# Optimization experiments

Hardware: AMD Instinct MI355X
Metric: run time of the kernel (lower is better)

Reference implementation:

```python
import jax, jax.numpy as jnp
import numpy as np

B, D, L, E, RH, EH = 8192, 1024, 3, 8, 128, 256  # batch, dim, levels, experts, router hidden, expert hidden


def setup_inputs() -> dict:
    key = jax.random.key(0)
    ks = jax.random.split(key, 9)
    s_d = 1.0 / np.sqrt(D)
    s_rh = 1.0 / np.sqrt(RH)
    s_eh = 1.0 / np.sqrt(EH)
    return {
        "x": jax.random.normal(ks[0], (B, D), dtype=jnp.float32),
        # routers: Linear(D,128) -> ReLU -> Linear(128,E) -> softmax, one per level
        "router_w1": jax.random.uniform(ks[1], (L, D, RH), jnp.float32, -s_d, s_d),
        "router_b1": jax.random.uniform(ks[2], (L, RH), jnp.float32, -s_d, s_d),
        "router_w2": jax.random.uniform(ks[3], (L, RH, E), jnp.float32, -s_rh, s_rh),
        "router_b2": jax.random.uniform(ks[4], (L, E), jnp.float32, -s_rh, s_rh),
        # experts: Linear(D,256) -> ReLU -> Linear(256,D), E per level
        "expert_w1": jax.random.uniform(ks[5], (L, E, D, EH), jnp.float32, -s_d, s_d),
        "expert_b1": jax.random.uniform(ks[6], (L, E, EH), jnp.float32, -s_d, s_d),
        "expert_w2": jax.random.uniform(ks[7], (L, E, EH, D), jnp.float32, -s_eh, s_eh),
        "expert_b2": jax.random.uniform(ks[8], (L, E, D), jnp.float32, -s_eh, s_eh),
    }


def _forward(x, router_w1, router_b1, router_w2, router_b2,
             expert_w1, expert_b1, expert_w2, expert_b2):
    def level(cur, params):
        rw1, rb1, rw2, rb2, ew1, eb1, ew2, eb2 = params
        # router: [B,E] softmax weights
        rh = jax.nn.relu(cur @ rw1 + rb1)
        w = jax.nn.softmax(rh @ rw2 + rb2, axis=-1)
        # dense all-expert eval: grouped GEMMs
        h = jax.nn.relu(jnp.einsum("bd,edh->beh", cur, ew1) + eb1)  # [B,E,EH]
        y = jnp.einsum("beh,ehd->bed", h, ew2) + eb2                # [B,E,D]
        out = jnp.einsum("be,bed->bd", w, y)                        # softmax-weighted sum
        return out, None

    out, _ = jax.lax.scan(
        level, x,
        (router_w1, router_b1, router_w2, router_b2,
         expert_w1, expert_b1, expert_w2, expert_b2))
    return out


def reference(x, router_w1, router_b1, router_w2, router_b2,
              expert_w1, expert_b1, expert_w2, expert_b2):
    return _forward(x, router_w1, router_b1, router_w2, router_b2,
                    expert_w1, expert_b1, expert_w2, expert_b2)
```

## Files before the change

### kernel.cpp

```cpp
#include <hip/hip_runtime.h>
#include <stdint.h>

#define BB   8192
#define DD   1024
#define EE   8
#define RHH  128
#define EHH  256
#define NE1  2048
#define KX   2112

using f32x4  = __attribute__((ext_vector_type(4))) float;
using bf16x8 = __attribute__((ext_vector_type(8))) __bf16;

__device__ __forceinline__ unsigned short f2bf(float f) {
    union { float f; uint32_t u; } v; v.f = f;
    uint32_t u = v.u;
    uint32_t r = (u + 0x7FFFu + ((u >> 16) & 1u)) >> 16;
    return (unsigned short)r;
}
__device__ __forceinline__ float bf2f(unsigned short h) {
    union { uint32_t u; float f; } v; v.u = ((uint32_t)h) << 16;
    return v.f;
}

__device__ __forceinline__ void llds16(void* l, const void* g) {
    __builtin_amdgcn_global_load_lds(
        (const __attribute__((address_space(1))) uint32_t*)g,
        (__attribute__((address_space(3))) uint32_t*)l, 16, 0, 0);
}

__device__ __forceinline__ void rawbar() {
    asm volatile("" ::: "memory");
    __builtin_amdgcn_s_barrier();
    asm volatile("" ::: "memory");
}

template<int N> __device__ __forceinline__ void vmwait() {
    asm volatile("s_waitcnt vmcnt(%0)" :: "n"(N) : "memory");
}


__device__ __forceinline__ void prep_body(int pbid, int tid,
    const float* __restrict__ rw1, const float* __restrict__ ew1,
    const float* __restrict__ ew2, const float* __restrict__ eb2,
    unsigned short* __restrict__ rw1t, unsigned short* __restrict__ W1t,
    unsigned short* __restrict__ W2t)
{
    if (pbid < 512) {
        int o = pbid * 256 + tid;
        int h = o >> 10, d = o & 1023;
        rw1t[o] = f2bf(rw1[d * RHH + h]);
    } else if (pbid < 8704) {
        int o = (pbid - 512) * 256 + tid;
        int n = o >> 10, k = o & 1023;
        int e = n >> 8, hh = n & 255;
        W1t[o] = f2bf(ew1[((e << 10) + k) * 256 + hh]);
    } else {
        int o = (pbid - 8704) * 256 + tid;
        int d = o / KX;
        int np = o - d * KX;
        float v;
        if (np < NE1)            v = ew2[np * DD + d];
        else if (np < NE1 + EE)  v = eb2[(np - NE1) * DD + d];
        else                     v = 0.0f;
        W2t[o] = f2bf(v);
    }
}

__global__ __launch_bounds__(256) void mega0(
    const float* __restrict__ x, unsigned short* __restrict__ xb,
    unsigned short* __restrict__ Hb,
    const float* __restrict__ rw1, const float* __restrict__ ew1,
    const float* __restrict__ ew2, const float* __restrict__ eb2,
    unsigned short* __restrict__ rw1t, unsigned short* __restrict__ W1t,
    unsigned short* __restrict__ W2t)
{
    const int bid = blockIdx.x, tid = threadIdx.x;
    if (bid < 2048) {
        size_t idx = (size_t)bid * 256 + tid;
        const float* p = x + idx * 16;
        uint32_t w[8];
#pragma unroll
        for (int j = 0; j < 8; ++j) {
            f32x4 v;
            (void)v;
            w[j] = (uint32_t)f2bf(p[2 * j]) | ((uint32_t)f2bf(p[2 * j + 1]) << 16);
        }
        uint32_t* o = (uint32_t*)(xb + idx * 16);
        *(uint4*)(o)     = make_uint4(w[0], w[1], w[2], w[3]);
        *(uint4*)(o + 4) = make_uint4(w[4], w[5], w[6], w[7]);
    } else if (bid < 3840) {
        int idx = (bid - 2048) * 256 + tid;
        int row = idx / 56, j = idx - row * 56;
        Hb[(size_t)row * KX + NE1 + EE + j] = 0;
    } else {
        prep_body(bid - 3840, tid, rw1, ew1, ew2, eb2, rw1t, W1t, W2t);
    }
}

__global__ __launch_bounds__(256) void prep_all(
    const float* __restrict__ rw1, const float* __restrict__ ew1,
    const float* __restrict__ ew2, const float* __restrict__ eb2,
    unsigned short* __restrict__ rw1t, unsigned short* __restrict__ W1t,
    unsigned short* __restrict__ W2t)
{
    prep_body(blockIdx.x, threadIdx.x, rw1, ew1, ew2, eb2, rw1t, W1t, W2t);
}

__global__ __launch_bounds__(512, 2) void router_fused(
    const unsigned short* __restrict__ xb, const unsigned short* __restrict__ rw1t,
    const float* __restrict__ rw2, const float* __restrict__ rb1,
    const float* __restrict__ rb2, float* __restrict__ wbuf,
    unsigned short* __restrict__ Hb)
{
    __shared__ __align__(16) char SR[73728];

    const int tid = threadIdx.x;
    const int lane = tid & 63, wv = tid >> 6;
    const int g = wv >> 2, wq = wv & 3;
    const int l16 = lane & 15, lhi = lane >> 4;
    const long m0 = (long)blockIdx.x * 64;

    const int r0 = tid >> 2, sl = tid & 3;
    const int sg = sl ^ ((r0 >> 1) & 3);

    const int xrow = (tid >> 2) & 63, xkg = tid >> 8;
    const char* xsrc = (const char*)xb + (m0 + xrow) * 2048 + xkg * 1024 + sg * 16;
    const char* wsrc = (const char*)rw1t + (long)r0 * 2048 + sg * 16;

    f32x4 acc[8];
    const f32x4 zero = {0.f, 0.f, 0.f, 0.f};
#pragma unroll
    for (int i = 0; i < 8; ++i) acc[i] = zero;

    auto stage = [&](int buf, int t) {
        char* base = SR + buf * 24576;
        llds16(base + tid * 16, xsrc + t * 64);
        llds16(base + 8192 + tid * 16, wsrc + t * 64);
        llds16(base + 16384 + tid * 16, wsrc + 1024 + t * 64);
    };

    stage(0, 0); stage(1, 1);

    const int swz = (l16 >> 1) & 3;
    const int aoff = g * 2048 + (wq * 16 + l16) * 32 + ((lhi ^ swz) << 3);
    const int boff = 4096 + g * 4096 + l16 * 32 + ((lhi ^ swz) << 3);

    int cb = 0, sb = 2;
    for (int t = 0; t < 16; ++t) {
        if (t < 15) vmwait<3>(); else vmwait<0>();
        rawbar();
        const unsigned short* bufp = (const unsigned short*)(SR + cb * 24576);
        bf16x8 aF = *(const bf16x8*)&bufp[aoff];
        bf16x8 bF[8];
#pragma unroll
        for (int ni = 0; ni < 8; ++ni)
            bF[ni] = *(const bf16x8*)&bufp[boff + ni * 512];
        if (t + 2 < 16) stage(sb, t + 2);
        __builtin_amdgcn_s_setprio(1);
#pragma unroll
        for (int ni = 0; ni < 8; ++ni)
            acc[ni] = __builtin_amdgcn_mfma_f32_16x16x32_bf16(aF, bF[ni], acc[ni], 0, 0, 0);
        __builtin_amdgcn_s_setprio(0);
        cb = (cb + 1 == 3) ? 0 : cb + 1;
        sb = (sb + 1 == 3) ? 0 : sb + 1;
    }

    rawbar();

    float* rhs = (float*)SR;
    float* lg  = (float*)(SR + 64 * 132 * 4);

    if (g == 1) {
#pragma unroll
        for (int ni = 0; ni < 8; ++ni)
#pragma unroll
            for (int rr = 0; rr < 4; ++rr)
                rhs[(wq * 16 + lhi * 4 + rr) * 132 + ni * 16 + l16] = acc[ni][rr];
    }
    rawbar();
    if (g == 0) {
#pragma unroll
        for (int ni = 0; ni < 8; ++ni) {
            float bv = rb1[ni * 16 + l16];
#pragma unroll
            for (int rr = 0; rr < 4; ++rr) {
                int row = wq * 16 + lhi * 4 + rr, col = ni * 16 + l16;
                float v = acc[ni][rr] + rhs[row * 132 + col] + bv;
                rhs[row * 132 + col] = fmaxf(v, 0.f);
            }
        }
    }
    rawbar();

    {
        const int row = tid & 63, e = tid >> 6;
        float a2 = rb2[e];
        for (int h = 0; h < 128; ++h)
            a2 += rhs[row * 132 + h] * rw2[h * 8 + e];
        lg[row * 9 + e] = a2;
    }
    rawbar();

    if (tid < 64) {
        const int row = tid;
        float l[8], m = -1e30f;
#pragma unroll
        for (int e = 0; e < 8; ++e) { l[e] = lg[row * 9 + e]; m = fmaxf(m, l[e]); }
        float s = 0.f;
#pragma unroll
        for (int e = 0; e < 8; ++e) { l[e] = expf(l[e] - m); s += l[e]; }
        float inv = 1.f / s;
        const long gr = m0 + row;
#pragma unroll
        for (int e = 0; e < 8; ++e) {
            float w = l[e] * inv;
            wbuf[gr * 8 + e] = w;
            Hb[gr * KX + NE1 + e] = f2bf(w);
        }
    }
}

template<int BNv, int BKv, int NBUF, int WNv, int EPI>
__global__ __launch_bounds__(512, 2)
void gemmT(const unsigned short* __restrict__ A, const unsigned short* __restrict__ Bt,
           void* __restrict__ C, const float* __restrict__ bias,
           const float* __restrict__ wrow,
           int K, int lda, int ldb, int ldc)
{
    constexpr int KH  = BKv / 32;
    constexpr int WMv = 8 / WNv;
    constexpr int MR  = 256 / WMv;
    constexpr int NC  = BNv / WNv;
    constexpr int MI  = MR / 16;
    constexpr int NI  = NC / 16;
    constexpr int NCH = 16 / MI;
    constexpr int ALP = 2;
    constexpr int BLP = (BNv * 64) / 8192;
    constexpr int LPT = KH * (ALP + BLP);
    constexpr int SD  = NBUF - 1;
    constexpr int AKH = 256 * 32;
    constexpr int BKH = BNv * 32;

    __shared__ __align__(16) unsigned short As[NBUF * KH * AKH];
    __shared__ __align__(16) unsigned short Bs[NBUF * KH * BKH];

    const int tid = threadIdx.x;
    const int lane = tid & 63, wv = tid >> 6;
    const int wr = wv / WNv, wc = wv % WNv;
    const int l16 = lane & 15, lhi = lane >> 4;
    const long bm0 = (long)blockIdx.x * 256;
    const long bn0 = (long)blockIdx.y * BNv;

    const int r0 = tid >> 2, sl = tid & 3;
    const int sg = sl ^ ((r0 >> 1) & 3);

    const char* aSrc[ALP];
    const char* bSrc[BLP];
#pragma unroll
    for (int a = 0; a < ALP; ++a)
        aSrc[a] = (const char*)A + (bm0 + a * 128 + r0) * (long)lda * 2 + sg * 16;
#pragma unroll
    for (int b = 0; b < BLP; ++b)
        bSrc[b] = (const char*)Bt + (bn0 + b * 128 + r0) * (long)ldb * 2 + sg * 16;

    f32x4 acc[MI][NI];
    const f32x4 zero = {0.f, 0.f, 0.f, 0.f};
#pragma unroll
    for (int i = 0; i < MI; ++i)
#pragma unroll
        for (int j = 0; j < NI; ++j)
            acc[i][j] = zero;

    auto stage = [&](int buf, int t) {
        const int cbyte = t * (BKv * 2);
#pragma unroll
        for (int kh = 0; kh < KH; ++kh) {
            char* ad = (char*)As + ((buf * KH + kh) * AKH) * 2 + tid * 16;
            char* bd = (char*)Bs + ((buf * KH + kh) * BKH) * 2 + tid * 16;
#pragma unroll
            for (int a = 0; a < ALP; ++a)
                llds16(ad + a * 8192, aSrc[a] + cbyte + kh * 64);
#pragma unroll
            for (int b = 0; b < BLP; ++b)
                llds16(bd + b * 8192, bSrc[b] + cbyte + kh * 64);
        }
    };

    const int nt = K / BKv;
#pragma unroll
    for (int p = 0; p < SD; ++p) stage(p, p);

    const int swz = (l16 >> 1) & 3;
    const int aoff = (wr * MR + l16) * 32 + ((lhi ^ swz) << 3);
    const int boff = (wc * NC + l16) * 32 + ((lhi ^ swz) << 3);

    int cb = 0, sb = SD % NBUF;
    for (int t = 0; t < nt; ++t) {
        const int rem = nt - 1 - t;
        if (rem >= SD - 1) vmwait<LPT * (SD - 1)>();
        else if constexpr (SD >= 3) {
            if (rem == 1) vmwait<LPT>(); else vmwait<0>();
        } else vmwait<0>();
        rawbar();

        bf16x8 aF[KH][MI], bF[KH][NI];
#pragma unroll
        for (int kh = 0; kh < KH; ++kh) {
            const unsigned short* ap = &As[(cb * KH + kh) * AKH];
            const unsigned short* bp = &Bs[(cb * KH + kh) * BKH];
#pragma unroll
            for (int mi = 0; mi < MI; ++mi)
                aF[kh][mi] = *(const bf16x8*)&ap[aoff + mi * 512];
#pragma unroll
            for (int ni = 0; ni < NI; ++ni)
                bF[kh][ni] = *(const bf16x8*)&bp[boff + ni * 512];
        }

        if (t + SD < nt) stage(sb, t + SD);

#pragma unroll
        for (int kh = 0; kh < KH; ++kh) {
#pragma unroll
            for (int nc0 = 0; nc0 < NI; nc0 += NCH) {
                __builtin_amdgcn_s_setprio(1);
#pragma unroll
                for (int mi = 0; mi < MI; ++mi)
#pragma unroll
                    for (int nj = 0; nj < NCH; ++nj)
                        acc[mi][nc0 + nj] = __builtin_amdgcn_mfma_f32_16x16x32_bf16(
                            aF[kh][mi], bF[kh][nc0 + nj], acc[mi][nc0 + nj], 0, 0, 0);
                __builtin_amdgcn_s_setprio(0);
            }
        }

        cb = (cb + 1 == NBUF) ? 0 : cb + 1;
        sb = (sb + 1 == NBUF) ? 0 : sb + 1;
    }

#pragma unroll
    for (int mi = 0; mi < MI; ++mi) {
#pragma unroll
        for (int ni = 0; ni < NI; ++ni) {
            const long gn = bn0 + wc * NC + ni * 16 + l16;
            float bv = 0.f;
            if (EPI == 1) bv = bias[gn];
#pragma unroll
            for (int rr = 0; rr < 4; ++rr) {
                const long gm = bm0 + wr * MR + mi * 16 + lhi * 4 + rr;
                float v = acc[mi][ni][rr];
                if (EPI == 1) {
                    v = fmaxf(v + bv, 0.f) * wrow[gm * 8 + (int)(gn >> 8)];
                    ((unsigned short*)C)[gm * (long)ldc + gn] = f2bf(v);
                } else if (EPI == 2) {
                    ((unsigned short*)C)[gm * (long)ldc + gn] = f2bf(v);
                } else {
                    ((float*)C)[gm * (long)ldc + gn] = v;
                }
            }
        }
    }
}


extern "C" void kernel_launch(void* const* d_in, const int* in_sizes, int n_in,
                              void* d_out, int out_size, void* d_ws, size_t ws_size,
                              hipStream_t stream) {
    (void)in_sizes; (void)n_in; (void)out_size; (void)ws_size;
    const float* x   = (const float*)d_in[0];
    const float* rw1 = (const float*)d_in[1];
    const float* rb1 = (const float*)d_in[2];
    const float* rw2 = (const float*)d_in[3];
    const float* rb2 = (const float*)d_in[4];
    const float* ew1 = (const float*)d_in[5];
    const float* eb1 = (const float*)d_in[6];
    const float* ew2 = (const float*)d_in[7];
    const float* eb2 = (const float*)d_in[8];

    char* ws = (char*)d_ws;
    unsigned short* xb   = (unsigned short*)(ws);
    float*          wbuf = (float*)         (ws + 16777216);
    unsigned short* Hb   = (unsigned short*)(ws + 17039360);
    unsigned short* rw1t = (unsigned short*)(ws + 51642368);
    unsigned short* W1t  = (unsigned short*)(ws + 51904512);
    unsigned short* W2t  = (unsigned short*)(ws + 56098816);

    mega0<<<20992, 256, 0, stream>>>(x, xb, Hb, rw1, ew1, ew2, eb2, rw1t, W1t, W2t);

    for (int l = 0; l < 3; ++l) {
        if (l > 0)
            prep_all<<<17152, 256, 0, stream>>>(rw1 + (size_t)l * DD * RHH,
                                                ew1 + (size_t)l * EE * DD * EHH,
                                                ew2 + (size_t)l * EE * EHH * DD,
                                                eb2 + (size_t)l * EE * DD,
                                                rw1t, W1t, W2t);

        router_fused<<<128, 512, 0, stream>>>(xb, rw1t,
                                              rw2 + (size_t)l * RHH * EE,
                                              rb1 + (size_t)l * RHH,
                                              rb2 + (size_t)l * EE, wbuf, Hb);

        gemmT<256, 32, 4, 4, 1><<<dim3(32, 8), 512, 0, stream>>>(
            xb, W1t, Hb, eb1 + (size_t)l * NE1, wbuf, DD, DD, DD, KX);

        if (l < 2)
            gemmT<128, 64, 3, 2, 2><<<dim3(32, 8), 512, 0, stream>>>(
                Hb, W2t, xb, nullptr, nullptr, KX, KX, KX, DD);
        else
            gemmT<128, 64, 3, 2, 3><<<dim3(32, 8), 512, 0, stream>>>(
                Hb, W2t, d_out, nullptr, nullptr, KX, KX, KX, DD);
    }
}
```

Before: 320.1 us.

## Replace GEMM mainloop with double-buffered, sub-tile interleaved load/compute schedule

Replaces the generic multi-buffer gemmT with gemmF. gemmF uses double buffering with BK=64 and splits each k-step into two or four MFMA phases. The refill of the freed LDS sub-tile (A or B halves) is issued between phases, with barriers and lgkmcnt waits placed explicitly. Warp layout is fixed at 2x4 with 128 rows per wave group, so the N=128 config moves from a 4x2 to a 2x4 wave arrangement. The aim is to overlap global->LDS traffic with MFMA work at finer granularity and cut LDS footprint. The cost is many more barriers per iteration and a fragile hand-written schedule.

```diff
diff --git a/kernel.cpp b/kernel.cpp
--- a/kernel.cpp
+++ b/kernel.cpp
@@ -38,6 +38,13 @@
 template<int N> __device__ __forceinline__ void vmwait() {
     asm volatile("s_waitcnt vmcnt(%0)" :: "n"(N) : "memory");
 }
+
+__device__ __forceinline__ void lgkm0sb() {
+    asm volatile("s_waitcnt lgkmcnt(0)" ::: "memory");
+    __builtin_amdgcn_sched_barrier(0);
+}
+
+#define MFMA16(a,b,c) __builtin_amdgcn_mfma_f32_16x16x32_bf16(a,b,c,0,0,0)
 
 
 __device__ __forceinline__ void prep_body(int pbid, int tid,
@@ -81,11 +88,8 @@
         const float* p = x + idx * 16;
         uint32_t w[8];
 #pragma unroll
-        for (int j = 0; j < 8; ++j) {
-            f32x4 v;
-            (void)v;
+        for (int j = 0; j < 8; ++j)
             w[j] = (uint32_t)f2bf(p[2 * j]) | ((uint32_t)f2bf(p[2 * j + 1]) << 16);
-        }
         uint32_t* o = (uint32_t*)(xb + idx * 16);
         *(uint4*)(o)     = make_uint4(w[0], w[1], w[2], w[3]);
         *(uint4*)(o + 4) = make_uint4(w[4], w[5], w[6], w[7]);
@@ -160,7 +164,7 @@
         __builtin_amdgcn_s_setprio(1);
 #pragma unroll
         for (int ni = 0; ni < 8; ++ni)
-            acc[ni] = __builtin_amdgcn_mfma_f32_16x16x32_bf16(aF, bF[ni], acc[ni], 0, 0, 0);
+            acc[ni] = MFMA16(aF, bF[ni], acc[ni]);
         __builtin_amdgcn_s_setprio(0);
         cb = (cb + 1 == 3) ? 0 : cb + 1;
         sb = (sb + 1 == 3) ? 0 : sb + 1;
@@ -221,125 +225,213 @@
     }
 }
 
-template<int BNv, int BKv, int NBUF, int WNv, int EPI>
+template<int BNv, int EPI>
 __global__ __launch_bounds__(512, 2)
-void gemmT(const unsigned short* __restrict__ A, const unsigned short* __restrict__ Bt,
+void gemmF(const unsigned short* __restrict__ A, const unsigned short* __restrict__ Bt,
            void* __restrict__ C, const float* __restrict__ bias,
            const float* __restrict__ wrow,
            int K, int lda, int ldb, int ldc)
 {
-    constexpr int KH  = BKv / 32;
-    constexpr int WMv = 8 / WNv;
-    constexpr int MR  = 256 / WMv;
-    constexpr int NC  = BNv / WNv;
-    constexpr int MI  = MR / 16;
+    constexpr int NC  = BNv / 4;
     constexpr int NI  = NC / 16;
-    constexpr int NCH = 16 / MI;
-    constexpr int ALP = 2;
-    constexpr int BLP = (BNv * 64) / 8192;
-    constexpr int LPT = KH * (ALP + BLP);
-    constexpr int SD  = NBUF - 1;
-    constexpr int AKH = 256 * 32;
     constexpr int BKH = BNv * 32;
 
-    __shared__ __align__(16) unsigned short As[NBUF * KH * AKH];
-    __shared__ __align__(16) unsigned short Bs[NBUF * KH * BKH];
+    __shared__ __align__(16) unsigned short As[2][16384];
+    __shared__ __align__(16) unsigned short Bs[2][2 * BKH];
 
     const int tid = threadIdx.x;
     const int lane = tid & 63, wv = tid >> 6;
-    const int wr = wv / WNv, wc = wv % WNv;
+    const int wr = wv >> 2, wc = wv & 3;
     const int l16 = lane & 15, lhi = lane >> 4;
+    const int lq = lane >> 2, ls = lane & 3;
+
     const long bm0 = (long)blockIdx.x * 256;
     const long bn0 = (long)blockIdx.y * BNv;
 
-    const int r0 = tid >> 2, sl = tid & 3;
-    const int sg = sl ^ ((r0 >> 1) & 3);
-
-    const char* aSrc[ALP];
-    const char* bSrc[BLP];
-#pragma unroll
-    for (int a = 0; a < ALP; ++a)
-        aSrc[a] = (const char*)A + (bm0 + a * 128 + r0) * (long)lda * 2 + sg * 16;
-#pragma unroll
-    for (int b = 0; b < BLP; ++b)
-        bSrc[b] = (const char*)Bt + (bn0 + b * 128 + r0) * (long)ldb * 2 + sg * 16;
-
-    f32x4 acc[MI][NI];
+    const int arb = (wv & 3) * 16 + (wv >> 2) * 128 + lq;
+    const int sgA = ls ^ ((arb >> 1) & 3);
+    const int brb = (BNv == 256) ? ((wv >> 1) * 64 + (wv & 1) * 16 + lq)
+                                 : (wv * 16 + lq);
+    const int sgB = ls ^ ((brb >> 1) & 3);
+
+    const char* aSrcU[2];
+    aSrcU[0] = (const char*)A + (bm0 + arb) * (long)lda * 2 + sgA * 16;
+    aSrcU[1] = aSrcU[0] + 64 * (long)lda * 2;
+    const char* bSrcU[2];
+    bSrcU[0] = (const char*)Bt + (bn0 + brb) * (long)ldb * 2 + sgB * 16;
+    bSrcU[1] = bSrcU[0] + 32 * (long)ldb * 2;
+
+    const int aDst0 = arb * 64 + ls * 16;
+    const int bDst0 = brb * 64 + ls * 16;
+
+    auto stA = [&](int buf, int mih, int t) {
+#pragma unroll
+        for (int g = 0; g < 2; ++g)
+            llds16((char*)As + buf * 32768 + g * 16384 + aDst0 + mih * 4096,
+                   aSrcU[mih] + (long)t * 128 + g * 64);
+    };
+    auto stB = [&](int buf, int nih, int t) {
+#pragma unroll
+        for (int g = 0; g < 2; ++g)
+            llds16((char*)Bs + buf * (4 * BKH) + g * (2 * BKH) + bDst0 + nih * 2048,
+                   bSrcU[nih] + (long)t * 128 + g * 64);
+    };
+
+    f32x4 acc[8][NI];
     const f32x4 zero = {0.f, 0.f, 0.f, 0.f};
 #pragma unroll
-    for (int i = 0; i < MI; ++i)
+    for (int i = 0; i < 8; ++i)
 #pragma unroll
         for (int j = 0; j < NI; ++j)
             acc[i][j] = zero;
 
-    auto stage = [&](int buf, int t) {
-        const int cbyte = t * (BKv * 2);
-#pragma unroll
-        for (int kh = 0; kh < KH; ++kh) {
-            char* ad = (char*)As + ((buf * KH + kh) * AKH) * 2 + tid * 16;
-            char* bd = (char*)Bs + ((buf * KH + kh) * BKH) * 2 + tid * 16;
-#pragma unroll
-            for (int a = 0; a < ALP; ++a)
-                llds16(ad + a * 8192, aSrc[a] + cbyte + kh * 64);
-#pragma unroll
-            for (int b = 0; b < BLP; ++b)
-                llds16(bd + b * 8192, bSrc[b] + cbyte + kh * 64);
+    const int swzo = (lhi ^ ((l16 >> 1) & 3)) << 3;
+    const int arow0 = (wr * 128 + l16) * 32 + swzo;
+    const int brow0 = (wc * NC + l16) * 32 + swzo;
+
+    const int nt = K / 64;
+
+    if constexpr (BNv == 256) {
+        stA(0, 0, 0); stA(0, 1, 0);
+        stB(0, 0, 0); stB(0, 1, 0);
+        stA(1, 0, 1); stA(1, 1, 1);
+    } else {
+        stB(0, 0, 0);
+        stA(0, 0, 0); stA(0, 1, 0);
+        stB(1, 0, 1);
+    }
+
+    bf16x8 aF[2][4], bF[2][NI];
+
+    for (int t = 0; t < nt; ++t) {
+        const int buf = t & 1;
+
+        if constexpr (BNv == 256) {
+            if (t == nt - 1) vmwait<0>(); else vmwait<4>();
+            rawbar();
+#pragma unroll
+            for (int kk = 0; kk < 2; ++kk)
+#pragma unroll
+                for (int mi = 0; mi < 4; ++mi)
+                    aF[kk][mi] = *(const bf16x8*)&As[buf][kk * 8192 + arow0 + mi * 512];
+#pragma unroll
+            for (int kk = 0; kk < 2; ++kk)
+#pragma unroll
+                for (int nj = 0; nj < 2; ++nj)
+                    bF[kk][nj] = *(const bf16x8*)&Bs[buf][kk * BKH + brow0 + nj * 512];
+            if (t + 1 < nt) stB(buf ^ 1, 0, t + 1);
+            lgkm0sb();
+            __builtin_amdgcn_s_setprio(1);
+#pragma unroll
+            for (int kk = 0; kk < 2; ++kk)
+#pragma unroll
+                for (int mi = 0; mi < 4; ++mi)
+#pragma unroll
+                    for (int nj = 0; nj < 2; ++nj)
+                        acc[mi][nj] = MFMA16(aF[kk][mi], bF[kk][nj], acc[mi][nj]);
+            __builtin_amdgcn_s_setprio(0);
+            rawbar();
+
+#pragma unroll
+            for (int kk = 0; kk < 2; ++kk)
+#pragma unroll
+                for (int nj = 0; nj < 2; ++nj)
+                    bF[kk][2 + nj] = *(const bf16x8*)&Bs[buf][kk * BKH + brow0 + (2 + nj) * 512];
+            if (t + 1 < nt) stB(buf ^ 1, 1, t + 1);
+            rawbar();
+            lgkm0sb();
+            __builtin_amdgcn_s_setprio(1);
+#pragma unroll
+            for (int kk = 0; kk < 2; ++kk)
+#pragma unroll
+                for (int mi = 0; mi < 4; ++mi)
+#pragma unroll
+                    for (int nj = 0; nj < 2; ++nj)
+                        acc[mi][2 + nj] = MFMA16(aF[kk][mi], bF[kk][2 + nj], acc[mi][2 + nj]);
+            __builtin_amdgcn_s_setprio(0);
+            rawbar();
+
+#pragma unroll
+            for (int kk = 0; kk < 2; ++kk)
+#pragma unroll
+                for (int mi = 0; mi < 4; ++mi)
+                    aF[kk][mi] = *(const bf16x8*)&As[buf][kk * 8192 + arow0 + 2048 + mi * 512];
+            if (t + 2 < nt) stA(buf, 0, t + 2);
+            rawbar();
+            lgkm0sb();
+            __builtin_amdgcn_s_setprio(1);
+#pragma unroll
+            for (int kk = 0; kk < 2; ++kk)
+#pragma unroll
+                for (int mi = 0; mi < 4; ++mi)
+#pragma unroll
+                    for (int nj = 0; nj < 2; ++nj)
+                        acc[4 + mi][nj] = MFMA16(aF[kk][mi], bF[kk][nj], acc[4 + mi][nj]);
+            __builtin_amdgcn_s_setprio(0);
+            rawbar();
+
+            if (t + 2 < nt) stA(buf, 1, t + 2);
+            rawbar();
+            lgkm0sb();
+            __builtin_amdgcn_s_setprio(1);
+#pragma unroll
+            for (int kk = 0; kk < 2; ++kk)
+#pragma unroll
+                for (int mi = 0; mi < 4; ++mi)
+#pragma unroll
+                    for (int nj = 0; nj < 2; ++nj)
+                        acc[4 + mi][2 + nj] = MFMA16(aF[kk][mi], bF[kk][2 + nj], acc[4 + mi][2 + nj]);
+            __builtin_amdgcn_s_setprio(0);
+            rawbar();
+        } else {
+            if (t == nt - 1) vmwait<0>(); else vmwait<2>();
+            rawbar();
+#pragma unroll
+            for (int kk = 0; kk < 2; ++kk)
+#pragma unroll
+                for (int mi = 0; mi < 4; ++mi)
+                    aF[kk][mi] = *(const bf16x8*)&As[buf][kk * 8192 + arow0 + mi * 512];
+#pragma unroll
+            for (int kk = 0; kk < 2; ++kk)
+#pragma unroll
+                for (int nj = 0; nj < 2; ++nj)
+                    bF[kk][nj] = *(const bf16x8*)&Bs[buf][kk * BKH + brow0 + nj * 512];
+            if (t + 1 < nt) { stA(buf ^ 1, 0, t + 1); stA(buf ^ 1, 1, t + 1); }
+            lgkm0sb();
+            __builtin_amdgcn_s_setprio(1);
+#pragma unroll
+            for (int kk = 0; kk < 2; ++kk)
+#pragma unroll
+                for (int mi = 0; mi < 4; ++mi)
+#pragma unroll
+                    for (int nj = 0; nj < 2; ++nj)
+                        acc[mi][nj] = MFMA16(aF[kk][mi], bF[kk][nj], acc[mi][nj]);
+            __builtin_amdgcn_s_setprio(0);
+            rawbar();
+
+#pragma unroll
+            for (int kk = 0; kk < 2; ++kk)
+#pragma unroll
+                for (int mi = 0; mi < 4; ++mi)
+                    aF[kk][mi] = *(const bf16x8*)&As[buf][kk * 8192 + arow0 + 2048 + mi * 512];
+            if (t + 2 < nt) stB(buf, 0, t + 2);
+            rawbar();
+            lgkm0sb();
+            __builtin_amdgcn_s_setprio(1);
+#pragma unroll
+            for (int kk = 0; kk < 2; ++kk)
+#pragma unroll
+                for (int mi = 0; mi < 4; ++mi)
+#pragma unroll
+                    for (int nj = 0; nj < 2; ++nj)
+                        acc[4 + mi][nj] = MFMA16(aF[kk][mi], bF[kk][nj], acc[4 + mi][nj]);
+            __builtin_amdgcn_s_setprio(0);
+            rawbar();
         }
-    };
-
-    const int nt = K / BKv;
-#pragma unroll
-    for (int p = 0; p < SD; ++p) stage(p, p);
-
-    const int swz = (l16 >> 1) & 3;
-    const int aoff = (wr * MR + l16) * 32 + ((lhi ^ swz) << 3);
-    const int boff = (wc * NC + l16) * 32 + ((lhi ^ swz) << 3);
-
-    int cb = 0, sb = SD % NBUF;
-    for (int t = 0; t < nt; ++t) {
-        const int rem = nt - 1 - t;
-        if (rem >= SD - 1) vmwait<LPT * (SD - 1)>();
-        else if constexpr (SD >= 3) {
-            if (rem == 1) vmwait<LPT>(); else vmwait<0>();
-        } else vmwait<0>();
-        rawbar();
-
-        bf16x8 aF[KH][MI], bF[KH][NI];
-#pragma unroll
-        for (int kh = 0; kh < KH; ++kh) {
-            const unsigned short* ap = &As[(cb * KH + kh) * AKH];
-            const unsigned short* bp = &Bs[(cb * KH + kh) * BKH];
-#pragma unroll
-            for (int mi = 0; mi < MI; ++mi)
-                aF[kh][mi] = *(const bf16x8*)&ap[aoff + mi * 512];
-#pragma unroll
-            for (int ni = 0; ni < NI; ++ni)
-                bF[kh][ni] = *(const bf16x8*)&bp[boff + ni * 512];
-        }
-
-        if (t + SD < nt) stage(sb, t + SD);
-
-#pragma unroll
-        for (int kh = 0; kh < KH; ++kh) {
-#pragma unroll
-            for (int nc0 = 0; nc0 < NI; nc0 += NCH) {
-                __builtin_amdgcn_s_setprio(1);
-#pragma unroll
-                for (int mi = 0; mi < MI; ++mi)
-#pragma unroll
-                    for (int nj = 0; nj < NCH; ++nj)
-                        acc[mi][nc0 + nj] = __builtin_amdgcn_mfma_f32_16x16x32_bf16(
-                            aF[kh][mi], bF[kh][nc0 + nj], acc[mi][nc0 + nj], 0, 0, 0);
-                __builtin_amdgcn_s_setprio(0);
-            }
-        }
-
-        cb = (cb + 1 == NBUF) ? 0 : cb + 1;
-        sb = (sb + 1 == NBUF) ? 0 : sb + 1;
-    }
-
-#pragma unroll
-    for (int mi = 0; mi < MI; ++mi) {
+    }
+
+#pragma unroll
+    for (int mi = 0; mi < 8; ++mi) {
 #pragma unroll
         for (int ni = 0; ni < NI; ++ni) {
             const long gn = bn0 + wc * NC + ni * 16 + l16;
@@ -347,7 +439,7 @@
             if (EPI == 1) bv = bias[gn];
 #pragma unroll
             for (int rr = 0; rr < 4; ++rr) {
-                const long gm = bm0 + wr * MR + mi * 16 + lhi * 4 + rr;
+                const long gm = bm0 + wr * 128 + mi * 16 + lhi * 4 + rr;
                 float v = acc[mi][ni][rr];
                 if (EPI == 1) {
                     v = fmaxf(v + bv, 0.f) * wrow[gm * 8 + (int)(gn >> 8)];
@@ -400,14 +492,14 @@
                                               rb1 + (size_t)l * RHH,
                                               rb2 + (size_t)l * EE, wbuf, Hb);
 
-        gemmT<256, 32, 4, 4, 1><<<dim3(32, 8), 512, 0, stream>>>(
+        gemmF<256, 1><<<dim3(32, 8), 512, 0, stream>>>(
             xb, W1t, Hb, eb1 + (size_t)l * NE1, wbuf, DD, DD, DD, KX);
 
         if (l < 2)
-            gemmT<128, 64, 3, 2, 2><<<dim3(32, 8), 512, 0, stream>>>(
+            gemmF<128, 2><<<dim3(32, 8), 512, 0, stream>>>(
                 Hb, W2t, xb, nullptr, nullptr, KX, KX, KX, DD);
         else
-            gemmT<128, 64, 3, 2, 3><<<dim3(32, 8), 512, 0, stream>>>(
+            gemmF<128, 3><<<dim3(32, 8), 512, 0, stream>>>(
                 Hb, W2t, d_out, nullptr, nullptr, KX, KX, KX, DD);
     }
 }
```

Measured after the change: 335.1 us. 1.05x slower.

## Replace generic GEMM with phase-scheduled ping-pong GEMMs using BK=128 stages

Applied to the files above, without the earlier changes.

Replaces the templated gemmT with two specialised kernels (256x256 and 256x128 tiles). Each K-step of 128 is split into barrier-delimited phases that interleave LDS fragment reads, global-to-LDS async loads and MFMA clusters over a double buffer. This is meant to hide load latency and keep the matrix units busy. To make the second GEMM's K a multiple of 128, the Hb padding grows from 2112 to 2176, which adds zero-fill work and shifts the workspace offsets. The risk is extra barriers and more padded K work.

```diff
diff --git a/kernel.cpp b/kernel.cpp
--- a/kernel.cpp
+++ b/kernel.cpp
@@ -7,7 +7,7 @@
 #define RHH  128
 #define EHH  256
 #define NE1  2048
-#define KX   2112
+#define KX   2176
 
 using f32x4  = __attribute__((ext_vector_type(4))) float;
 using bf16x8 = __attribute__((ext_vector_type(8))) __bf16;
@@ -38,6 +38,20 @@
 template<int N> __device__ __forceinline__ void vmwait() {
     asm volatile("s_waitcnt vmcnt(%0)" :: "n"(N) : "memory");
 }
+
+#define MFMA16(a,b,c) __builtin_amdgcn_mfma_f32_16x16x32_bf16(a,b,c,0,0,0)
+
+#define PH_MID() do { rawbar(); \
+    asm volatile("s_waitcnt lgkmcnt(0)" ::: "memory"); \
+    __builtin_amdgcn_s_setprio(1); } while (0)
+#define PH_END() do { __builtin_amdgcn_s_setprio(0); rawbar(); } while (0)
+#define PH_END_VM(N) do { __builtin_amdgcn_s_setprio(0); vmwait<N>(); rawbar(); } while (0)
+
+#define CLUST(AM, AN, AF, BF)                            \
+    _Pragma("unroll") for (int kk = 0; kk < 2; ++kk)     \
+    _Pragma("unroll") for (int mi = 0; mi < 4; ++mi)     \
+    _Pragma("unroll") for (int nj = 0; nj < 2; ++nj)     \
+        acc[(AM) + mi][(AN) + nj] = MFMA16(AF[kk][mi], BF[kk][nj], acc[(AM) + mi][(AN) + nj]);
 
 
 __device__ __forceinline__ void prep_body(int pbid, int tid,
@@ -81,20 +95,17 @@
         const float* p = x + idx * 16;
         uint32_t w[8];
 #pragma unroll
-        for (int j = 0; j < 8; ++j) {
-            f32x4 v;
-            (void)v;
+        for (int j = 0; j < 8; ++j)
             w[j] = (uint32_t)f2bf(p[2 * j]) | ((uint32_t)f2bf(p[2 * j + 1]) << 16);
-        }
         uint32_t* o = (uint32_t*)(xb + idx * 16);
         *(uint4*)(o)     = make_uint4(w[0], w[1], w[2], w[3]);
         *(uint4*)(o + 4) = make_uint4(w[4], w[5], w[6], w[7]);
-    } else if (bid < 3840) {
+    } else if (bid < 5888) {
         int idx = (bid - 2048) * 256 + tid;
-        int row = idx / 56, j = idx - row * 56;
+        int row = idx / 120, j = idx - row * 120;
         Hb[(size_t)row * KX + NE1 + EE + j] = 0;
     } else {
-        prep_body(bid - 3840, tid, rw1, ew1, ew2, eb2, rw1t, W1t, W2t);
+        prep_body(bid - 5888, tid, rw1, ew1, ew2, eb2, rw1t, W1t, W2t);
     }
 }
 
@@ -160,7 +171,7 @@
         __builtin_amdgcn_s_setprio(1);
 #pragma unroll
         for (int ni = 0; ni < 8; ++ni)
-            acc[ni] = __builtin_amdgcn_mfma_f32_16x16x32_bf16(aF, bF[ni], acc[ni], 0, 0, 0);
+            acc[ni] = MFMA16(aF, bF[ni], acc[ni]);
         __builtin_amdgcn_s_setprio(0);
         cb = (cb + 1 == 3) ? 0 : cb + 1;
         sb = (sb + 1 == 3) ? 0 : sb + 1;
@@ -221,145 +232,248 @@
     }
 }
 
-template<int BNv, int BKv, int NBUF, int WNv, int EPI>
+template<int EPI>
 __global__ __launch_bounds__(512, 2)
-void gemmT(const unsigned short* __restrict__ A, const unsigned short* __restrict__ Bt,
-           void* __restrict__ C, const float* __restrict__ bias,
-           const float* __restrict__ wrow,
-           int K, int lda, int ldb, int ldc)
+void gemm256(const unsigned short* __restrict__ A, const unsigned short* __restrict__ Bt,
+             void* __restrict__ C, const float* __restrict__ bias,
+             const float* __restrict__ wrow,
+             int K, int lda, int ldb, int ldc)
 {
-    constexpr int KH  = BKv / 32;
-    constexpr int WMv = 8 / WNv;
-    constexpr int MR  = 256 / WMv;
-    constexpr int NC  = BNv / WNv;
-    constexpr int MI  = MR / 16;
-    constexpr int NI  = NC / 16;
-    constexpr int NCH = 16 / MI;
-    constexpr int ALP = 2;
-    constexpr int BLP = (BNv * 64) / 8192;
-    constexpr int LPT = KH * (ALP + BLP);
-    constexpr int SD  = NBUF - 1;
-    constexpr int AKH = 256 * 32;
-    constexpr int BKH = BNv * 32;
-
-    __shared__ __align__(16) unsigned short As[NBUF * KH * AKH];
-    __shared__ __align__(16) unsigned short Bs[NBUF * KH * BKH];
+    __shared__ __align__(16) unsigned short As[2][16384];
+    __shared__ __align__(16) unsigned short Bs[2][16384];
 
     const int tid = threadIdx.x;
     const int lane = tid & 63, wv = tid >> 6;
-    const int wr = wv / WNv, wc = wv % WNv;
+    const int wr = wv >> 2, wc = wv & 3;
     const int l16 = lane & 15, lhi = lane >> 4;
+    const int lq = lane >> 2, ls = lane & 3;
+
     const long bm0 = (long)blockIdx.x * 256;
-    const long bn0 = (long)blockIdx.y * BNv;
-
-    const int r0 = tid >> 2, sl = tid & 3;
-    const int sg = sl ^ ((r0 >> 1) & 3);
-
-    const char* aSrc[ALP];
-    const char* bSrc[BLP];
-#pragma unroll
-    for (int a = 0; a < ALP; ++a)
-        aSrc[a] = (const char*)A + (bm0 + a * 128 + r0) * (long)lda * 2 + sg * 16;
-#pragma unroll
-    for (int b = 0; b < BLP; ++b)
-        bSrc[b] = (const char*)Bt + (bn0 + b * 128 + r0) * (long)ldb * 2 + sg * 16;
-
-    f32x4 acc[MI][NI];
+    const long bn0 = (long)blockIdx.y * 256;
+
+    const int arb = (wv & 3) * 16 + (wv >> 2) * 128 + lq;
+    const int sgA = ls ^ ((arb >> 1) & 3);
+    const int brb = (wv >> 1) * 64 + (wv & 1) * 16 + lq;
+    const int sgB = ls ^ ((brb >> 1) & 3);
+
+    const char* aSrcU[2];
+    aSrcU[0] = (const char*)A + (bm0 + arb) * (long)lda * 2 + sgA * 16;
+    aSrcU[1] = aSrcU[0] + 64 * (long)lda * 2;
+    const char* bSrcU[2];
+    bSrcU[0] = (const char*)Bt + (bn0 + brb) * (long)ldb * 2 + sgB * 16;
+    bSrcU[1] = bSrcU[0] + 32 * (long)ldb * 2;
+
+    const int aDst0 = arb * 64 + ls * 16;
+    const int bDst0 = brb * 64 + ls * 16;
+
+    auto stA = [&](int buf, int mih, int t) {
+#pragma unroll
+        for (int g = 0; g < 2; ++g)
+            llds16((char*)As + buf * 32768 + g * 16384 + aDst0 + mih * 4096,
+                   aSrcU[mih] + (long)t * 128 + g * 64);
+    };
+    auto stB = [&](int buf, int nih, int t) {
+#pragma unroll
+        for (int g = 0; g < 2; ++g)
+            llds16((char*)Bs + buf * 32768 + g * 16384 + bDst0 + nih * 2048,
+                   bSrcU[nih] + (long)t * 128 + g * 64);
+    };
+
+    f32x4 acc[8][4];
     const f32x4 zero = {0.f, 0.f, 0.f, 0.f};
 #pragma unroll
-    for (int i = 0; i < MI; ++i)
-#pragma unroll
-        for (int j = 0; j < NI; ++j)
+    for (int i = 0; i < 8; ++i)
+#pragma unroll
+        for (int j = 0; j < 4; ++j)
             acc[i][j] = zero;
 
-    auto stage = [&](int buf, int t) {
-        const int cbyte = t * (BKv * 2);
-#pragma unroll
-        for (int kh = 0; kh < KH; ++kh) {
-            char* ad = (char*)As + ((buf * KH + kh) * AKH) * 2 + tid * 16;
-            char* bd = (char*)Bs + ((buf * KH + kh) * BKH) * 2 + tid * 16;
-#pragma unroll
-            for (int a = 0; a < ALP; ++a)
-                llds16(ad + a * 8192, aSrc[a] + cbyte + kh * 64);
-#pragma unroll
-            for (int b = 0; b < BLP; ++b)
-                llds16(bd + b * 8192, bSrc[b] + cbyte + kh * 64);
-        }
-    };
-
-    const int nt = K / BKv;
-#pragma unroll
-    for (int p = 0; p < SD; ++p) stage(p, p);
-
-    const int swz = (l16 >> 1) & 3;
-    const int aoff = (wr * MR + l16) * 32 + ((lhi ^ swz) << 3);
-    const int boff = (wc * NC + l16) * 32 + ((lhi ^ swz) << 3);
-
-    int cb = 0, sb = SD % NBUF;
-    for (int t = 0; t < nt; ++t) {
-        const int rem = nt - 1 - t;
-        if (rem >= SD - 1) vmwait<LPT * (SD - 1)>();
-        else if constexpr (SD >= 3) {
-            if (rem == 1) vmwait<LPT>(); else vmwait<0>();
-        } else vmwait<0>();
-        rawbar();
-
-        bf16x8 aF[KH][MI], bF[KH][NI];
-#pragma unroll
-        for (int kh = 0; kh < KH; ++kh) {
-            const unsigned short* ap = &As[(cb * KH + kh) * AKH];
-            const unsigned short* bp = &Bs[(cb * KH + kh) * BKH];
-#pragma unroll
-            for (int mi = 0; mi < MI; ++mi)
-                aF[kh][mi] = *(const bf16x8*)&ap[aoff + mi * 512];
-#pragma unroll
-            for (int ni = 0; ni < NI; ++ni)
-                bF[kh][ni] = *(const bf16x8*)&bp[boff + ni * 512];
-        }
-
-        if (t + SD < nt) stage(sb, t + SD);
-
-#pragma unroll
-        for (int kh = 0; kh < KH; ++kh) {
-#pragma unroll
-            for (int nc0 = 0; nc0 < NI; nc0 += NCH) {
-                __builtin_amdgcn_s_setprio(1);
-#pragma unroll
-                for (int mi = 0; mi < MI; ++mi)
-#pragma unroll
-                    for (int nj = 0; nj < NCH; ++nj)
-                        acc[mi][nc0 + nj] = __builtin_amdgcn_mfma_f32_16x16x32_bf16(
-                            aF[kh][mi], bF[kh][nc0 + nj], acc[mi][nc0 + nj], 0, 0, 0);
-                __builtin_amdgcn_s_setprio(0);
-            }
-        }
-
-        cb = (cb + 1 == NBUF) ? 0 : cb + 1;
-        sb = (sb + 1 == NBUF) ? 0 : sb + 1;
-    }
-
-#pragma unroll
-    for (int mi = 0; mi < MI; ++mi) {
-#pragma unroll
-        for (int ni = 0; ni < NI; ++ni) {
-            const long gn = bn0 + wc * NC + ni * 16 + l16;
-            float bv = 0.f;
-            if (EPI == 1) bv = bias[gn];
+    const int swzo = (lhi ^ ((l16 >> 1) & 3)) << 3;
+    const int arow0 = (wr * 128 + l16) * 32 + swzo;
+    const int brow0 = (wc * 64 + l16) * 32 + swzo;
+
+#define RD_A6(DST, BUF, MIH)                                  \
+    _Pragma("unroll") for (int kk = 0; kk < 2; ++kk)          \
+    _Pragma("unroll") for (int mi = 0; mi < 4; ++mi)          \
+        DST[kk][mi] = *(const bf16x8*)&As[BUF][kk * 8192 + arow0 + (MIH) * 2048 + mi * 512];
+#define RD_B6(DST, BUF, NIH)                                  \
+    _Pragma("unroll") for (int kk = 0; kk < 2; ++kk)          \
+    _Pragma("unroll") for (int nj = 0; nj < 2; ++nj)          \
+        DST[kk][nj] = *(const bf16x8*)&Bs[BUF][kk * 8192 + brow0 + ((NIH) * 2 + nj) * 512];
+
+    bf16x8 aF[2][4], bn0F[2][2], bn1F[2][2];
+
+    stA(0, 0, 0); stB(0, 0, 0); stB(0, 1, 0); stA(0, 1, 0);
+    stA(1, 0, 1); stB(1, 0, 1); stB(1, 1, 1);
+    vmwait<6>(); rawbar();
+
+    const int nI = K / 128;
+    for (int i = 0; i < nI; ++i) {
+        const int t = 2 * i;
+        const bool last = (i == nI - 1);
+
+        RD_A6(aF, 0, 0);
+        RD_B6(bn0F, 0, 0);
+        stA(1, 1, t + 1);
+        PH_MID(); CLUST(0, 0, aF, bn0F); PH_END();
+        RD_B6(bn1F, 0, 1);
+        if (!last) stA(0, 0, t + 2);
+        PH_MID(); CLUST(0, 2, aF, bn1F); PH_END();
+        RD_A6(aF, 0, 1);
+        if (!last) stB(0, 0, t + 2);
+        PH_MID(); CLUST(4, 2, aF, bn1F); PH_END();
+        if (!last) stB(0, 1, t + 2);
+        PH_MID(); CLUST(4, 0, aF, bn0F);
+        if (last) { PH_END_VM(0); } else { PH_END_VM(6); }
+        RD_A6(aF, 1, 0);
+        RD_B6(bn0F, 1, 0);
+        if (!last) stA(0, 1, t + 2);
+        PH_MID(); CLUST(0, 0, aF, bn0F); PH_END();
+        RD_B6(bn1F, 1, 1);
+        if (!last) stA(1, 0, t + 3);
+        PH_MID(); CLUST(0, 2, aF, bn1F); PH_END();
+        RD_A6(aF, 1, 1);
+        if (!last) stB(1, 0, t + 3);
+        PH_MID(); CLUST(4, 2, aF, bn1F); PH_END();
+        if (!last) stB(1, 1, t + 3);
+        PH_MID(); CLUST(4, 0, aF, bn0F);
+        if (!last) { PH_END_VM(6); }
+        else       { __builtin_amdgcn_s_setprio(0); }
+    }
+
+#pragma unroll
+    for (int mi = 0; mi < 8; ++mi) {
+#pragma unroll
+        for (int ni = 0; ni < 4; ++ni) {
+            const long gn = bn0 + wc * 64 + ni * 16 + l16;
+            float bv = (EPI == 1) ? bias[gn] : 0.f;
 #pragma unroll
             for (int rr = 0; rr < 4; ++rr) {
-                const long gm = bm0 + wr * MR + mi * 16 + lhi * 4 + rr;
+                const long gm = bm0 + wr * 128 + mi * 16 + lhi * 4 + rr;
                 float v = acc[mi][ni][rr];
                 if (EPI == 1) {
                     v = fmaxf(v + bv, 0.f) * wrow[gm * 8 + (int)(gn >> 8)];
                     ((unsigned short*)C)[gm * (long)ldc + gn] = f2bf(v);
-                } else if (EPI == 2) {
+                } else {
                     ((unsigned short*)C)[gm * (long)ldc + gn] = f2bf(v);
-                } else {
-                    ((float*)C)[gm * (long)ldc + gn] = v;
                 }
             }
         }
     }
+#undef RD_A6
+#undef RD_B6
+}
+
+template<int EPI>
+__global__ __launch_bounds__(512, 2)
+void gemm128(const unsigned short* __restrict__ A, const unsigned short* __restrict__ Bt,
+             void* __restrict__ C, int K, int lda, int ldb, int ldc)
+{
+    __shared__ __align__(16) unsigned short As[2][16384];
+    __shared__ __align__(16) unsigned short Bs[2][8192];
+
+    const int tid = threadIdx.x;
+    const int lane = tid & 63, wv = tid >> 6;
+    const int wr = wv >> 2, wc = wv & 3;
+    const int l16 = lane & 15, lhi = lane >> 4;
+    const int lq = lane >> 2, ls = lane & 3;
+
+    const long bm0 = (long)blockIdx.x * 256;
+    const long bn0 = (long)blockIdx.y * 128;
+
+    const int arb = (wv & 3) * 16 + (wv >> 2) * 128 + lq;
+    const int sgA = ls ^ ((arb >> 1) & 3);
+    const int brb = wv * 16 + lq;
+    const int sgB = ls ^ ((brb >> 1) & 3);
+
+    const char* aSrcU[2];
+    aSrcU[0] = (const char*)A + (bm0 + arb) * (long)lda * 2 + sgA * 16;
+    aSrcU[1] = aSrcU[0] + 64 * (long)lda * 2;
+    const char* bSrc = (const char*)Bt + (bn0 + brb) * (long)ldb * 2 + sgB * 16;
+
+    const int aDst0 = arb * 64 + ls * 16;
+    const int bDst0 = brb * 64 + ls * 16;
+
+    auto stA = [&](int buf, int mih, int t) {
+#pragma unroll
+        for (int g = 0; g < 2; ++g)
+            llds16((char*)As + buf * 32768 + g * 16384 + aDst0 + mih * 4096,
+                   aSrcU[mih] + (long)t * 128 + g * 64);
+    };
+    auto stB2 = [&](int buf, int t) {
+#pragma unroll
+        for (int g = 0; g < 2; ++g)
+            llds16((char*)Bs + buf * 16384 + g * 8192 + bDst0,
+                   bSrc + (long)t * 128 + g * 64);
+    };
+
+    f32x4 acc[8][2];
+    const f32x4 zero = {0.f, 0.f, 0.f, 0.f};
+#pragma unroll
+    for (int i = 0; i < 8; ++i)
+#pragma unroll
+        for (int j = 0; j < 2; ++j)
+            acc[i][j] = zero;
+
+    const int swzo = (lhi ^ ((l16 >> 1) & 3)) << 3;
+    const int arow0 = (wr * 128 + l16) * 32 + swzo;
+    const int brow0 = (wc * 32 + l16) * 32 + swzo;
+
+#define RD_A4(DST, BUF, MIH)                                  \
+    _Pragma("unroll") for (int kk = 0; kk < 2; ++kk)          \
+    _Pragma("unroll") for (int mi = 0; mi < 4; ++mi)          \
+        DST[kk][mi] = *(const bf16x8*)&As[BUF][kk * 8192 + arow0 + (MIH) * 2048 + mi * 512];
+#define RD_B4(DST, BUF)                                       \
+    _Pragma("unroll") for (int kk = 0; kk < 2; ++kk)          \
+    _Pragma("unroll") for (int nj = 0; nj < 2; ++nj)          \
+        DST[kk][nj] = *(const bf16x8*)&Bs[BUF][kk * 4096 + brow0 + nj * 512];
+
+    bf16x8 aF[2][4], bF[2][2];
+
+    stA(0, 0, 0); stB2(0, 0); stA(0, 1, 0);
+    stA(1, 0, 1); stB2(1, 1);
+    vmwait<6>(); rawbar();
+
+    const int nI = K / 128;
+    for (int i = 0; i < nI; ++i) {
+        const int t = 2 * i;
+        const bool last = (i == nI - 1);
+
+        RD_A4(aF, 0, 0);
+        RD_B4(bF, 0);
+        stA(1, 1, t + 1);
+        PH_MID(); CLUST(0, 0, aF, bF); PH_END_VM(6);
+        RD_A4(aF, 0, 1);
+        if (!last) { stA(0, 0, t + 2); stB2(0, t + 2); }
+        PH_MID(); CLUST(4, 0, aF, bF);
+        if (last) { PH_END_VM(2); } else { PH_END_VM(6); }
+        RD_A4(aF, 1, 0);
+        RD_B4(bF, 1);
+        if (!last) stA(0, 1, t + 2);
+        PH_MID(); CLUST(0, 0, aF, bF);
+        if (last) { PH_END_VM(0); } else { PH_END_VM(6); }
+        RD_A4(aF, 1, 1);
+        if (!last) { stA(1, 0, t + 3); stB2(1, t + 3); }
+        PH_MID(); CLUST(4, 0, aF, bF);
+        if (!last) { PH_END_VM(6); }
+        else       { __builtin_amdgcn_s_setprio(0); }
+    }
+
+#pragma unroll
+    for (int mi = 0; mi < 8; ++mi) {
+#pragma unroll
+        for (int ni = 0; ni < 2; ++ni) {
+            const long gn = bn0 + wc * 32 + ni * 16 + l16;
+#pragma unroll
+            for (int rr = 0; rr < 4; ++rr) {
+                const long gm = bm0 + wr * 128 + mi * 16 + lhi * 4 + rr;
+                float v = acc[mi][ni][rr];
+                if (EPI == 2) ((unsigned short*)C)[gm * (long)ldc + gn] = f2bf(v);
+                else          ((float*)C)[gm * (long)ldc + gn] = v;
+            }
+        }
+    }
+#undef RD_A4
+#undef RD_B4
 }
 
 
@@ -381,15 +495,15 @@
     unsigned short* xb   = (unsigned short*)(ws);
     float*          wbuf = (float*)         (ws + 16777216);
     unsigned short* Hb   = (unsigned short*)(ws + 17039360);
-    unsigned short* rw1t = (unsigned short*)(ws + 51642368);
-    unsigned short* W1t  = (unsigned short*)(ws + 51904512);
-    unsigned short* W2t  = (unsigned short*)(ws + 56098816);
-
-    mega0<<<20992, 256, 0, stream>>>(x, xb, Hb, rw1, ew1, ew2, eb2, rw1t, W1t, W2t);
+    unsigned short* rw1t = (unsigned short*)(ws + 52690944);
+    unsigned short* W1t  = (unsigned short*)(ws + 52953088);
+    unsigned short* W2t  = (unsigned short*)(ws + 57147392);
+
+    mega0<<<23296, 256, 0, stream>>>(x, xb, Hb, rw1, ew1, ew2, eb2, rw1t, W1t, W2t);
 
     for (int l = 0; l < 3; ++l) {
         if (l > 0)
-            prep_all<<<17152, 256, 0, stream>>>(rw1 + (size_t)l * DD * RHH,
+            prep_all<<<17408, 256, 0, stream>>>(rw1 + (size_t)l * DD * RHH,
                                                 ew1 + (size_t)l * EE * DD * EHH,
                                                 ew2 + (size_t)l * EE * EHH * DD,
                                                 eb2 + (size_t)l * EE * DD,
@@ -400,14 +514,14 @@
                                               rb1 + (size_t)l * RHH,
                                               rb2 + (size_t)l * EE, wbuf, Hb);
 
-        gemmT<256, 32, 4, 4, 1><<<dim3(32, 8), 512, 0, stream>>>(
+        gemm256<1><<<dim3(32, 8), 512, 0, stream>>>(
             xb, W1t, Hb, eb1 + (size_t)l * NE1, wbuf, DD, DD, DD, KX);
 
         if (l < 2)
-            gemmT<128, 64, 3, 2, 2><<<dim3(32, 8), 512, 0, stream>>>(
-                Hb, W2t, xb, nullptr, nullptr, KX, KX, KX, DD);
+            gemm128<2><<<dim3(32, 8), 512, 0, stream>>>(
+                Hb, W2t, xb, KX, KX, KX, DD);
         else
-            gemmT<128, 64, 3, 2, 3><<<dim3(32, 8), 512, 0, stream>>>(
-                Hb, W2t, d_out, nullptr, nullptr, KX, KX, KX, DD);
-    }
-}
+            gemm128<3><<<dim3(32, 8), 512, 0, stream>>>(
+                Hb, W2t, d_out, KX, KX, KX, DD);
+    }
+}
```

Result: slower. 346.2 us (+8.2%).

## Tile weight-prep transposes through shared memory and vectorize padding writes

Applied to the files above, without the earlier changes.

Replaces the per-element strided transpose-and-convert of expert and router weights with 64x64 tiles staged through padded shared memory, so both the global reads and the bf16 writes are coalesced. Padding zeroing and the eb2 bias columns are now written as 16-byte vector stores, which cuts the prep grid from tens of thousands of blocks to about a thousand. The GEMM main loop also issues the next stage's async loads before reading fragments from LDS, for extra overlap. Each block now uses a small shared buffer and a barrier, and the loop reorder changes when buffer reuse happens relative to the LDS reads.

```diff
diff --git a/kernel.cpp b/kernel.cpp
--- a/kernel.cpp
+++ b/kernel.cpp
@@ -39,31 +39,72 @@
     asm volatile("s_waitcnt vmcnt(%0)" :: "n"(N) : "memory");
 }
 
-
-__device__ __forceinline__ void prep_body(int pbid, int tid,
+#define MFMA16(a,b,c) __builtin_amdgcn_mfma_f32_16x16x32_bf16(a,b,c,0,0,0)
+
+__device__ __forceinline__ void prep_lvl_body(float (*T)[65], int pbid, int tid,
     const float* __restrict__ rw1, const float* __restrict__ ew1,
     const float* __restrict__ ew2, const float* __restrict__ eb2,
     unsigned short* __restrict__ rw1t, unsigned short* __restrict__ W1t,
     unsigned short* __restrict__ W2t)
 {
+    const int hl = tid & 63, gq = tid >> 6;
     if (pbid < 512) {
-        int o = pbid * 256 + tid;
-        int h = o >> 10, d = o & 1023;
-        rw1t[o] = f2bf(rw1[d * RHH + h]);
-    } else if (pbid < 8704) {
-        int o = (pbid - 512) * 256 + tid;
-        int n = o >> 10, k = o & 1023;
-        int e = n >> 8, hh = n & 255;
-        W1t[o] = f2bf(ew1[((e << 10) + k) * 256 + hh]);
+        int e = pbid >> 6, kt = (pbid >> 2) & 15, ht = pbid & 3;
+        const float* src = ew1 + ((size_t)e << 18);
+#pragma unroll
+        for (int i = 0; i < 16; ++i) {
+            int kl = i * 4 + gq;
+            T[kl][hl] = src[(size_t)(kt * 64 + kl) * 256 + ht * 64 + hl];
+        }
+        __syncthreads();
+#pragma unroll
+        for (int i = 0; i < 16; ++i) {
+            int hl2 = i * 4 + gq;
+            int n = e * 256 + ht * 64 + hl2;
+            W1t[(size_t)n * 1024 + kt * 64 + hl] = f2bf(T[hl][hl2]);
+        }
+    } else if (pbid < 1024) {
+        int b2 = pbid - 512;
+        int npt = b2 >> 4, dt = b2 & 15;
+#pragma unroll
+        for (int i = 0; i < 16; ++i) {
+            int npl = i * 4 + gq;
+            T[npl][hl] = ew2[(size_t)(npt * 64 + npl) * 1024 + dt * 64 + hl];
+        }
+        __syncthreads();
+#pragma unroll
+        for (int i = 0; i < 16; ++i) {
+            int dl2 = i * 4 + gq;
+            int d = dt * 64 + dl2;
+            W2t[(size_t)d * KX + npt * 64 + hl] = f2bf(T[hl][dl2]);
+        }
+    } else if (pbid < 1056) {
+        int b2 = pbid - 1024;
+        int dt = b2 >> 1, ht = b2 & 1;
+#pragma unroll
+        for (int i = 0; i < 16; ++i) {
+            int dl = i * 4 + gq;
+            T[dl][hl] = rw1[(size_t)(dt * 64 + dl) * 128 + ht * 64 + hl];
+        }
+        __syncthreads();
+#pragma unroll
+        for (int i = 0; i < 16; ++i) {
+            int hl2 = i * 4 + gq;
+            int h = ht * 64 + hl2;
+            rw1t[(size_t)h * 1024 + dt * 64 + hl] = f2bf(T[hl][hl2]);
+        }
+    } else if (pbid < 1060) {
+        int d = (pbid - 1056) * 256 + tid;
+        unsigned short vv[8];
+#pragma unroll
+        for (int e = 0; e < 8; ++e) vv[e] = f2bf(eb2[(size_t)e * 1024 + d]);
+        *(uint4*)&W2t[(size_t)d * KX + NE1] = *(const uint4*)vv;
     } else {
-        int o = (pbid - 8704) * 256 + tid;
-        int d = o / KX;
-        int np = o - d * KX;
-        float v;
-        if (np < NE1)            v = ew2[np * DD + d];
-        else if (np < NE1 + EE)  v = eb2[(np - NE1) * DD + d];
-        else                     v = 0.0f;
-        W2t[o] = f2bf(v);
+        int d = (pbid - 1060) * 256 + tid;
+        uint4 z = make_uint4(0, 0, 0, 0);
+#pragma unroll
+        for (int j = 0; j < 7; ++j)
+            *(uint4*)&W2t[(size_t)d * KX + NE1 + 8 + j * 8] = z;
     }
 }
 
@@ -75,36 +116,38 @@
     unsigned short* __restrict__ rw1t, unsigned short* __restrict__ W1t,
     unsigned short* __restrict__ W2t)
 {
+    __shared__ float T[64][65];
     const int bid = blockIdx.x, tid = threadIdx.x;
     if (bid < 2048) {
         size_t idx = (size_t)bid * 256 + tid;
         const float* p = x + idx * 16;
         uint32_t w[8];
 #pragma unroll
-        for (int j = 0; j < 8; ++j) {
-            f32x4 v;
-            (void)v;
+        for (int j = 0; j < 8; ++j)
             w[j] = (uint32_t)f2bf(p[2 * j]) | ((uint32_t)f2bf(p[2 * j + 1]) << 16);
-        }
         uint32_t* o = (uint32_t*)(xb + idx * 16);
         *(uint4*)(o)     = make_uint4(w[0], w[1], w[2], w[3]);
         *(uint4*)(o + 4) = make_uint4(w[4], w[5], w[6], w[7]);
-    } else if (bid < 3840) {
-        int idx = (bid - 2048) * 256 + tid;
-        int row = idx / 56, j = idx - row * 56;
-        Hb[(size_t)row * KX + NE1 + EE + j] = 0;
+    } else if (bid < 2080) {
+        int row = (bid - 2048) * 256 + tid;
+        uint4 z = make_uint4(0, 0, 0, 0);
+        unsigned short* p = Hb + (size_t)row * KX + NE1 + EE;
+#pragma unroll
+        for (int j = 0; j < 7; ++j)
+            *(uint4*)(p + j * 8) = z;
     } else {
-        prep_body(bid - 3840, tid, rw1, ew1, ew2, eb2, rw1t, W1t, W2t);
-    }
-}
-
-__global__ __launch_bounds__(256) void prep_all(
+        prep_lvl_body(T, bid - 2080, tid, rw1, ew1, ew2, eb2, rw1t, W1t, W2t);
+    }
+}
+
+__global__ __launch_bounds__(256) void prep_lvl(
     const float* __restrict__ rw1, const float* __restrict__ ew1,
     const float* __restrict__ ew2, const float* __restrict__ eb2,
     unsigned short* __restrict__ rw1t, unsigned short* __restrict__ W1t,
     unsigned short* __restrict__ W2t)
 {
-    prep_body(blockIdx.x, threadIdx.x, rw1, ew1, ew2, eb2, rw1t, W1t, W2t);
+    __shared__ float T[64][65];
+    prep_lvl_body(T, blockIdx.x, threadIdx.x, rw1, ew1, ew2, eb2, rw1t, W1t, W2t);
 }
 
 __global__ __launch_bounds__(512, 2) void router_fused(
@@ -160,7 +203,7 @@
         __builtin_amdgcn_s_setprio(1);
 #pragma unroll
         for (int ni = 0; ni < 8; ++ni)
-            acc[ni] = __builtin_amdgcn_mfma_f32_16x16x32_bf16(aF, bF[ni], acc[ni], 0, 0, 0);
+            acc[ni] = MFMA16(aF, bF[ni], acc[ni]);
         __builtin_amdgcn_s_setprio(0);
         cb = (cb + 1 == 3) ? 0 : cb + 1;
         sb = (sb + 1 == 3) ? 0 : sb + 1;
@@ -304,6 +347,8 @@
         } else vmwait<0>();
         rawbar();
 
+        if (t + SD < nt) stage(sb, t + SD);
+
         bf16x8 aF[KH][MI], bF[KH][NI];
 #pragma unroll
         for (int kh = 0; kh < KH; ++kh) {
@@ -317,8 +362,6 @@
                 bF[kh][ni] = *(const bf16x8*)&bp[boff + ni * 512];
         }
 
-        if (t + SD < nt) stage(sb, t + SD);
-
 #pragma unroll
         for (int kh = 0; kh < KH; ++kh) {
 #pragma unroll
@@ -328,8 +371,8 @@
                 for (int mi = 0; mi < MI; ++mi)
 #pragma unroll
                     for (int nj = 0; nj < NCH; ++nj)
-                        acc[mi][nc0 + nj] = __builtin_amdgcn_mfma_f32_16x16x32_bf16(
-                            aF[kh][mi], bF[kh][nc0 + nj], acc[mi][nc0 + nj], 0, 0, 0);
+                        acc[mi][nc0 + nj] = MFMA16(aF[kh][mi], bF[kh][nc0 + nj],
+                                                   acc[mi][nc0 + nj]);
                 __builtin_amdgcn_s_setprio(0);
             }
         }
@@ -385,15 +428,15 @@
     unsigned short* W1t  = (unsigned short*)(ws + 51904512);
     unsigned short* W2t  = (unsigned short*)(ws + 56098816);
 
-    mega0<<<20992, 256, 0, stream>>>(x, xb, Hb, rw1, ew1, ew2, eb2, rw1t, W1t, W2t);
+    mega0<<<3144, 256, 0, stream>>>(x, xb, Hb, rw1, ew1, ew2, eb2, rw1t, W1t, W2t);
 
     for (int l = 0; l < 3; ++l) {
         if (l > 0)
-            prep_all<<<17152, 256, 0, stream>>>(rw1 + (size_t)l * DD * RHH,
-                                                ew1 + (size_t)l * EE * DD * EHH,
-                                                ew2 + (size_t)l * EE * EHH * DD,
-                                                eb2 + (size_t)l * EE * DD,
-                                                rw1t, W1t, W2t);
+            prep_lvl<<<1064, 256, 0, stream>>>(rw1 + (size_t)l * DD * RHH,
+                                               ew1 + (size_t)l * EE * DD * EHH,
+                                               ew2 + (size_t)l * EE * EHH * DD,
+                                               eb2 + (size_t)l * EE * DD,
+                                               rw1t, W1t, W2t);
 
         router_fused<<<128, 512, 0, stream>>>(xb, rw1t,
                                               rw2 + (size_t)l * RHH * EE,
```

Result: slower. 364.9 us (+14.0%).
